# Kernel optimization log

Hardware: AMD Instinct MI355X
Metric: run time of the kernel (lower is better)

Reference implementation:

```python
import jax, jax.numpy as jnp
import numpy as np

B, T, C, H = 8, 2048, 1024, 128  # batch, seq (== block_size), n_embd, head_size


def setup_inputs() -> dict:
    key = jax.random.key(0)
    ks = jax.random.split(key, 4)
    s = 1.0 / np.sqrt(C)  # keep logits sane for softmax
    return {
        "embedded_data": jax.random.normal(ks[0], (B, T, C), dtype=jnp.float32),
        "Wq": jax.random.normal(ks[1], (C, H), dtype=jnp.float32) * s,
        "bq": jnp.zeros((H,), dtype=jnp.float32),
        "Wk": jax.random.normal(ks[2], (C, H), dtype=jnp.float32) * s,
        "bk": jnp.zeros((H,), dtype=jnp.float32),
        "Wv": jax.random.normal(ks[3], (C, H), dtype=jnp.float32) * s,
        "bv": jnp.zeros((H,), dtype=jnp.float32),
    }


def reference(embedded_data, Wq, bq, Wk, bk, Wv, bv):
    Bc, Tc, Cc = embedded_data.shape
    q = embedded_data @ Wq + bq                      # [B,T,H]
    k = embedded_data @ Wk + bk                      # [B,T,H]
    v = embedded_data @ Wv + bv                      # [B,T,H]
    # NOTE: source scales by C**-0.5 (input embed dim), not head_size**-0.5
    wei = jnp.einsum("bqh,bkh->bqk", q, k) * (Cc ** -0.5)  # [B,T,T]
    causal = jnp.tril(jnp.ones((Tc, Tc), dtype=bool))
    wei = jnp.where(causal, wei, -jnp.inf)
    wei = jax.nn.softmax(wei, axis=-1)
    # dropout(p=0.2) is identity in eval mode
    out = jnp.einsum("bqk,bkh->bqh", wei, v)         # [B,T,H]
    return out
```

## Files before the change

kernel.cpp:

```cpp
#include <hip/hip_runtime.h>
#include <cstdint>
#include <cstddef>

typedef __bf16 bf16x8 __attribute__((ext_vector_type(8)));
typedef float f32x4 __attribute__((ext_vector_type(4)));

#define B_ 8
#define T_ 2048
#define C_ 1024
#define H_ 128

#define QSC 0.045084220027780106f

__device__ __forceinline__ unsigned short f2bf(float f) {
    __bf16 h = (__bf16)f;
    return *(unsigned short*)&h;
}
__device__ __forceinline__ float bf2f(unsigned short u) {
    union { unsigned int i; float f; } x; x.i = ((unsigned int)u) << 16;
    return x.f;
}

__device__ __forceinline__ void gload16(void* lds, const void* g) {
    __builtin_amdgcn_global_load_lds(
        (const __attribute__((address_space(1))) unsigned int*)g,
        (__attribute__((address_space(3))) unsigned int*)lds, 16, 0, 0);
}

__global__ __launch_bounds__(256) void prep_w(
    const float* __restrict__ Wq, const float* __restrict__ Wk,
    const float* __restrict__ Wv, unsigned short* __restrict__ wt)
{
    int gid = blockIdx.x * 256 + threadIdx.x;
    int which = gid >> 14;
    int rem = gid & 16383;
    int n = rem >> 7;
    int kc = rem & 127;
    const float* W = which == 0 ? Wq : (which == 1 ? Wk : Wv);
    unsigned short tmp[8];
    #pragma unroll
    for (int i = 0; i < 8; ++i) tmp[i] = f2bf(W[(size_t)(kc * 8 + i) * H_ + n]);
    *(uint4*)&wt[((size_t)which * H_ + n) * C_ + kc * 8] = *(uint4*)tmp;
}

__global__ __launch_bounds__(256, 2) void proj_fused5(
    const float* __restrict__ x, const unsigned short* __restrict__ wt,
    const float* __restrict__ bq, const float* __restrict__ bk,
    const float* __restrict__ bv,
    unsigned short* __restrict__ qo, unsigned short* __restrict__ ko,
    unsigned short* __restrict__ vo)
{
    __shared__ unsigned short smem[32768];

    const int tid = threadIdx.x;
    const int w = tid >> 6, l = tid & 63, gl = l >> 4, lc = l & 15;
    const int cb = w * 48;
    const int fam = blockIdx.y;
    const int m0 = blockIdx.x * 64;
    const unsigned short* wbase = wt + (size_t)fam * 192 * C_;

    const int sr = tid >> 2, q4 = tid & 3;
    const float* xrow = &x[(size_t)(m0 + sr) * C_ + q4 * 16];
    unsigned short* xw0;
    unsigned short* xw1;
    {
        int c0 = q4 * 2;
        (void)c0;
    }

    f32x4 acc[4][3];
    #pragma unroll
    for (int im = 0; im < 4; ++im)
        #pragma unroll
        for (int jn = 0; jn < 3; ++jn) acc[im][jn] = f32x4{0.f, 0.f, 0.f, 0.f};

    float xr[16];
    auto load_x = [&](int kc2) {
        const float* p = xrow + kc2 * 64;
        #pragma unroll
        for (int i = 0; i < 4; ++i) {
            float4 v4 = *(const float4*)(p + 4 * i);
            xr[4 * i + 0] = v4.x; xr[4 * i + 1] = v4.y;
            xr[4 * i + 2] = v4.z; xr[4 * i + 3] = v4.w;
        }
    };
    auto write_x = [&](int buf) {
        unsigned short tb[16];
        #pragma unroll
        for (int i = 0; i < 16; ++i) tb[i] = f2bf(xr[i]);
        unsigned short* xb = smem + buf * 4096;
        const int c0 = q4 * 2;
        *(uint4*)&xb[(sr * 8 + ((c0 + 0) ^ (sr & 7))) * 8] = *(uint4*)&tb[0];
        *(uint4*)&xb[(sr * 8 + ((c0 + 1) ^ (sr & 7))) * 8] = *(uint4*)&tb[8];
    };
    auto stage_w = [&](int buf, int kc2) {
        const int kb = kc2 * 64;
        unsigned short* wb = smem + 8192 + buf * 12288;
        #pragma unroll
        for (int ji = 0; ji < 6; ++ji) {
            int slot = ji * 256 + tid;
            int R = slot >> 3, cs = slot & 7;
            gload16(&wb[(ji * 256 + w * 64) * 8],
                    &wbase[(size_t)R * C_ + kb + ((cs ^ (R & 7)) * 8)]);
        }
    };

    load_x(0);
    stage_w(0, 0);
    asm volatile("s_waitcnt vmcnt(6)" ::: "memory");
    __builtin_amdgcn_sched_barrier(0);
    write_x(0);
    load_x(1);
    stage_w(1, 1);
    asm volatile("s_waitcnt vmcnt(10)" ::: "memory");
    __builtin_amdgcn_sched_barrier(0);
    asm volatile("s_waitcnt lgkmcnt(0)" ::: "memory");
    __builtin_amdgcn_sched_barrier(0);
    __builtin_amdgcn_s_barrier();

    for (int kc = 0; kc < 16; ++kc) {
        const int cur = kc & 1, nxt = cur ^ 1;
        const unsigned short* xb = smem + cur * 4096;
        const unsigned short* wb = smem + 8192 + cur * 12288;
        #pragma unroll
        for (int ks = 0; ks < 2; ++ks) {
            bf16x8 a[4], b[3];
            const int u = ks * 4 + gl;
            #pragma unroll
            for (int im = 0; im < 4; ++im) {
                int row = im * 16 + lc;
                a[im] = *(const bf16x8*)&xb[(row * 8 + (u ^ (lc & 7))) * 8];
            }
            #pragma unroll
            for (int jn = 0; jn < 3; ++jn) {
                int R = cb + jn * 16 + lc;
                b[jn] = *(const bf16x8*)&wb[(R * 8 + (u ^ (lc & 7))) * 8];
            }
            #pragma unroll
            for (int im = 0; im < 4; ++im)
                #pragma unroll
                for (int jn = 0; jn < 3; ++jn)
                    acc[im][jn] = __builtin_amdgcn_mfma_f32_16x16x32_bf16(
                        a[im], b[jn], acc[im][jn], 0, 0, 0);
        }
        __builtin_amdgcn_s_barrier();
        if (kc < 14) {
            asm volatile("s_waitcnt vmcnt(6)" ::: "memory");
            __builtin_amdgcn_sched_barrier(0);
            write_x(nxt);
            load_x(kc + 2);
            stage_w(cur, kc + 2);
            asm volatile("s_waitcnt vmcnt(10)" ::: "memory");
            __builtin_amdgcn_sched_barrier(0);
            asm volatile("s_waitcnt lgkmcnt(0)" ::: "memory");
            __builtin_amdgcn_sched_barrier(0);
            __builtin_amdgcn_s_barrier();
        } else if (kc == 14) {
            asm volatile("s_waitcnt vmcnt(6)" ::: "memory");
            __builtin_amdgcn_sched_barrier(0);
            write_x(nxt);
            asm volatile("s_waitcnt vmcnt(0)" ::: "memory");
            __builtin_amdgcn_sched_barrier(0);
            asm volatile("s_waitcnt lgkmcnt(0)" ::: "memory");
            __builtin_amdgcn_sched_barrier(0);
            __builtin_amdgcn_s_barrier();
        }
    }

    unsigned short* eb = smem;
    #pragma unroll
    for (int jn = 0; jn < 3; ++jn) {
        int nl_ = cb + jn * 16 + lc;
        int ng = fam * 192 + nl_;
        int wh = ng >> 7, nn = ng & 127;
        float bb = (wh == 0) ? bq[nn] : (wh == 1 ? bk[nn] : bv[nn]);
        float sc = (wh == 0) ? QSC : 1.0f;
        #pragma unroll
        for (int im = 0; im < 4; ++im)
            #pragma unroll
            for (int r = 0; r < 4; ++r) {
                int row = im * 16 + gl * 4 + r;
                eb[row * 200 + nl_] = f2bf((acc[im][jn][r] + bb) * sc);
            }
    }
    __syncthreads();

    const int bi = m0 >> 11, t0 = m0 & (T_ - 1);
    if (fam == 0) {
        #pragma unroll
        for (int i = 0; i < 4; ++i) {
            int c = i * 256 + tid;
            int row = c >> 4, c16 = c & 15;
            *(uint4*)&qo[(size_t)(m0 + row) * H_ + c16 * 8] =
                *(const uint4*)&eb[row * 200 + c16 * 8];
        }
        #pragma unroll
        for (int i = 0; i < 2; ++i) {
            int c = i * 256 + tid;
            int row = c >> 3, c8 = c & 7;
            *(uint4*)&ko[(size_t)(m0 + row) * H_ + c8 * 8] =
                *(const uint4*)&eb[row * 200 + 128 + c8 * 8];
        }
    } else {
        #pragma unroll
        for (int i = 0; i < 2; ++i) {
            int c = i * 256 + tid;
            int row = c >> 3, c8 = c & 7;
            *(uint4*)&ko[(size_t)(m0 + row) * H_ + 64 + c8 * 8] =
                *(const uint4*)&eb[row * 200 + c8 * 8];
        }
        #pragma unroll
        for (int i = 0; i < 4; ++i) {
            int c = i * 256 + tid;
            int n = c >> 3, cc = c & 7;
            unsigned short tmp[8];
            #pragma unroll
            for (int ii = 0; ii < 8; ++ii)
                tmp[ii] = eb[(cc * 8 + ii) * 200 + 64 + n];
            *(uint4*)&vo[((size_t)(bi * H_ + n)) * T_ + t0 + cc * 8] = *(uint4*)tmp;
        }
    }
}

__device__ __forceinline__ int pasc(int qt) {
    int m = qt >> 2, j = qt & 3;
    return 2 * m * (m + 1) + j * (m + 1);
}

__global__ __launch_bounds__(256, 2) void attn_split7(
    const unsigned short* __restrict__ q,
    const unsigned short* __restrict__ k,
    const unsigned short* __restrict__ vT,
    float* __restrict__ out,
    unsigned short* __restrict__ Opart, float* __restrict__ lws)
{
    const int bb = blockIdx.x;
    const int jj = 143 - (int)blockIdx.y;
    int qt = 31;
    while (pasc(qt) > jj) --qt;
    const int c = jj - pasc(qt);
    const int nch = (qt >> 2) + 1;
    const int q0 = qt * 64;
    const int kstart = c * 256;
    const int kend = min(kstart + 256, q0 + 64);
    const int ntiles = (kend - kstart) >> 5;

    const unsigned short* qb = q  + (size_t)bb * T_ * H_;
    const unsigned short* kb = k  + (size_t)bb * T_ * H_;
    const unsigned short* vb = vT + (size_t)bb * H_ * T_;

    __shared__ unsigned short Ks[2][32 * 128];
    __shared__ unsigned short Vs[2][128 * 32];
    __shared__ unsigned short Ps[4][16 * 64];

    const int tid = threadIdx.x;
    const int w = tid >> 6, l = tid & 63, gl = l >> 4, lc = l & 15;
    const int rowbase = q0 + w * 16;

    bf16x8 aq[4];
    #pragma unroll
    for (int ds = 0; ds < 4; ++ds)
        aq[ds] = *(const bf16x8*)&qb[(size_t)(rowbase + lc) * H_ + ds * 32 + gl * 8];

    f32x4 o[8];
    #pragma unroll
    for (int jo = 0; jo < 8; ++jo) o[jo] = f32x4{0.f, 0.f, 0.f, 0.f};
    float l_acc[4];
    #pragma unroll
    for (int r = 0; r < 4; ++r) l_acc[r] = 0.f;

    auto stageK = [&](int buf, int t) {
        const int kv0 = kstart + t * 32;
        #pragma unroll
        for (int ji = 0; ji < 2; ++ji) {
            int slot = (w * 2 + ji) * 64 + l;
            int r = slot >> 4, cs = slot & 15;
            gload16(&Ks[buf][((w * 2 + ji) * 64) * 8],
                    &kb[(size_t)(kv0 + r) * H_ + ((cs ^ (r & 7)) * 8)]);
        }
    };
    auto stageV = [&](int buf, int t) {
        const int kv0 = kstart + t * 32;
        #pragma unroll
        for (int ji = 0; ji < 2; ++ji) {
            int slot = (w * 2 + ji) * 64 + l;
            int r = slot >> 2, cs = slot & 3;
            gload16(&Vs[buf][((w * 2 + ji) * 64) * 8],
                    &vb[(size_t)r * T_ + kv0 + ((cs ^ (r & 3)) * 8)]);
        }
    };

    stageK(0, 0);
    stageV(0, 0);
    __syncthreads();

    int cur = 0;
    for (int t = 0; t < ntiles; ++t) {
        if (t + 1 < ntiles) { stageK(cur ^ 1, t + 1); stageV(cur ^ 1, t + 1); }
        const int kv0 = kstart + t * 32;
        const bool active = kv0 < rowbase + 16;
        if (active) {
            f32x4 s[2];
            #pragma unroll
            for (int jk = 0; jk < 2; ++jk) s[jk] = f32x4{0.f, 0.f, 0.f, 0.f};
            #pragma unroll
            for (int ds = 0; ds < 4; ++ds) {
                #pragma unroll
                for (int jk = 0; jk < 2; ++jk) {
                    int row = jk * 16 + lc;
                    bf16x8 kf = *(const bf16x8*)&Ks[cur][(row * 16 + ((ds * 4 + gl) ^ (row & 7))) * 8];
                    s[jk] = __builtin_amdgcn_mfma_f32_16x16x32_bf16(aq[ds], kf, s[jk], 0, 0, 0);
                }
            }
            if (kv0 + 31 > rowbase) {
                #pragma unroll
                for (int jk = 0; jk < 2; ++jk)
                    #pragma unroll
                    for (int r = 0; r < 4; ++r)
                        if (kv0 + jk * 16 + lc > rowbase + gl * 4 + r) s[jk][r] = -1e30f;
            }
            #pragma unroll
            for (int jk = 0; jk < 2; ++jk)
                #pragma unroll
                for (int r = 0; r < 4; ++r) {
                    float p = exp2f(fminf(s[jk][r], 80.f));
                    s[jk][r] = p;
                    l_acc[r] += p;
                }
            #pragma unroll
            for (int jk = 0; jk < 2; ++jk)
                #pragma unroll
                for (int r = 0; r < 4; ++r) {
                    int row = gl * 4 + r;
                    Ps[w][(row * 64 + jk * 16 + lc) ^ ((row & 7) << 3)] = f2bf(s[jk][r]);
                }
            {
                bf16x8 pa = *(const bf16x8*)&Ps[w][(lc * 64 + gl * 8) ^ ((lc & 7) << 3)];
                #pragma unroll
                for (int jo = 0; jo < 8; ++jo) {
                    int d = jo * 16 + lc;
                    bf16x8 vf = *(const bf16x8*)&Vs[cur][(d * 4 + (gl ^ (d & 3))) * 8];
                    o[jo] = __builtin_amdgcn_mfma_f32_16x16x32_bf16(pa, vf, o[jo], 0, 0, 0);
                }
            }
        }
        __syncthreads();
        cur ^= 1;
    }

    #pragma unroll
    for (int off = 1; off < 16; off <<= 1)
        #pragma unroll
        for (int r = 0; r < 4; ++r)
            l_acc[r] += __shfl_xor(l_acc[r], off, 64);

    if (nch == 1) {
        float* ob = out + (size_t)bb * T_ * H_;
        float inv[4];
        #pragma unroll
        for (int r = 0; r < 4; ++r) inv[r] = 1.0f / l_acc[r];
        #pragma unroll
        for (int jo = 0; jo < 8; ++jo)
            #pragma unroll
            for (int r = 0; r < 4; ++r)
                ob[(size_t)(rowbase + gl * 4 + r) * H_ + jo * 16 + lc] = o[jo][r] * inv[r];
    } else {
        const int slot = bb * 140 + (pasc(qt) - 4 + c);
        unsigned short* op = Opart + (size_t)slot * 8192;
        #pragma unroll
        for (int jo = 0; jo < 8; ++jo)
            #pragma unroll
            for (int r = 0; r < 4; ++r)
                op[(w * 16 + gl * 4 + r) * 128 + jo * 16 + lc] = f2bf(o[jo][r]);
        if (lc == 0) {
            #pragma unroll
            for (int r = 0; r < 4; ++r)
                lws[slot * 64 + w * 16 + gl * 4 + r] = l_acc[r];
        }
    }
}

__global__ __launch_bounds__(256) void combine_kernel(
    const unsigned short* __restrict__ Opart, const float* __restrict__ lws,
    float* __restrict__ out)
{
    const int rowid = blockIdx.x * 4 + (threadIdx.x >> 6);
    const int lane = threadIdx.x & 63;
    const int bb = rowid / 1792;
    const int t = 256 + (rowid - bb * 1792);
    const int qt = t >> 6;
    const int m = qt >> 2;
    const int nch = m + 1;
    const int p0 = 2 * m * (m + 1) + (qt & 3) * (m + 1);
    const int base = bb * 140 + (p0 - 4);
    const int r64 = t & 63;

    float L = 0.f, a0 = 0.f, a1 = 0.f;
    #pragma unroll
    for (int c2 = 0; c2 < 8; ++c2)
        if (c2 < nch) {
            L += lws[(base + c2) * 64 + r64];
            ushort2 uv = *(const ushort2*)&Opart[(size_t)(base + c2) * 8192 + r64 * 128 + lane * 2];
            a0 += bf2f(uv.x); a1 += bf2f(uv.y);
        }
    const float invL = 1.0f / L;
    *(float2*)&out[((size_t)bb * T_ + t) * H_ + lane * 2] = make_float2(a0 * invL, a1 * invL);
}

__global__ __launch_bounds__(128) void attn_mono(
    const unsigned short* __restrict__ q,
    const unsigned short* __restrict__ k,
    const unsigned short* __restrict__ vT,
    float* __restrict__ out)
{
    const int qt = (gridDim.x - 1) - blockIdx.x;
    const int bb = blockIdx.y;
    const int q0 = qt * 32;
    const unsigned short* qb = q  + (size_t)bb * T_ * H_;
    const unsigned short* kb = k  + (size_t)bb * T_ * H_;
    const unsigned short* vb = vT + (size_t)bb * H_ * T_;

    __shared__ unsigned short Ps[2][16 * 64];

    const int tid = threadIdx.x;
    const int w = tid >> 6, l = tid & 63, gl = l >> 4, lc = l & 15;

    bf16x8 aq[4];
    #pragma unroll
    for (int ds = 0; ds < 4; ++ds)
        aq[ds] = *(const bf16x8*)&qb[(size_t)(q0 + w * 16 + lc) * H_ + ds * 32 + gl * 8];

    f32x4 o[8];
    #pragma unroll
    for (int jo = 0; jo < 8; ++jo) o[jo] = f32x4{0.f, 0.f, 0.f, 0.f};
    float m_run[4], l_run[4];
    #pragma unroll
    for (int r = 0; r < 4; ++r) { m_run[r] = -INFINITY; l_run[r] = 0.f; }

    const int nt = (q0 >> 6) + 1;
    for (int t = 0; t < nt; ++t) {
        const int kv0 = t * 64;
        f32x4 s[4];
        #pragma unroll
        for (int jk = 0; jk < 4; ++jk) s[jk] = f32x4{0.f, 0.f, 0.f, 0.f};
        #pragma unroll
        for (int ds = 0; ds < 4; ++ds)
            #pragma unroll
            for (int jk = 0; jk < 4; ++jk) {
                bf16x8 bf = *(const bf16x8*)&kb[(size_t)(kv0 + jk * 16 + lc) * H_ + ds * 32 + gl * 8];
                s[jk] = __builtin_amdgcn_mfma_f32_16x16x32_bf16(aq[ds], bf, s[jk], 0, 0, 0);
            }
        if (kv0 + 63 > q0) {
            const int rowg = q0 + w * 16 + gl * 4;
            #pragma unroll
            for (int jk = 0; jk < 4; ++jk)
                #pragma unroll
                for (int r = 0; r < 4; ++r)
                    if (kv0 + jk * 16 + lc > rowg + r) s[jk][r] = -1e30f;
        }
        float pm[4];
        #pragma unroll
        for (int r = 0; r < 4; ++r)
            pm[r] = fmaxf(fmaxf(s[0][r], s[1][r]), fmaxf(s[2][r], s[3][r]));
        #pragma unroll
        for (int off = 1; off < 16; off <<= 1)
            #pragma unroll
            for (int r = 0; r < 4; ++r)
                pm[r] = fmaxf(pm[r], __shfl_xor(pm[r], off, 64));
        float scl[4], rs[4];
        #pragma unroll
        for (int r = 0; r < 4; ++r) {
            float mn = fmaxf(m_run[r], pm[r]);
            scl[r] = exp2f(m_run[r] - mn);
            m_run[r] = mn;
            rs[r] = 0.f;
        }
        #pragma unroll
        for (int jk = 0; jk < 4; ++jk)
            #pragma unroll
            for (int r = 0; r < 4; ++r) {
                float p = exp2f(s[jk][r] - m_run[r]);
                s[jk][r] = p;
                rs[r] += p;
            }
        #pragma unroll
        for (int off = 1; off < 16; off <<= 1)
            #pragma unroll
            for (int r = 0; r < 4; ++r)
                rs[r] += __shfl_xor(rs[r], off, 64);
        #pragma unroll
        for (int r = 0; r < 4; ++r)
            l_run[r] = l_run[r] * scl[r] + rs[r];
        #pragma unroll
        for (int jo = 0; jo < 8; ++jo)
            #pragma unroll
            for (int r = 0; r < 4; ++r)
                o[jo][r] *= scl[r];
        #pragma unroll
        for (int jk = 0; jk < 4; ++jk)
            #pragma unroll
            for (int r = 0; r < 4; ++r) {
                int row = gl * 4 + r;
                Ps[w][(row * 64 + jk * 16 + lc) ^ ((row & 7) << 3)] = f2bf(s[jk][r]);
            }
        #pragma unroll
        for (int ks = 0; ks < 2; ++ks) {
            bf16x8 pa = *(const bf16x8*)&Ps[w][(lc * 64 + ks * 32 + gl * 8) ^ ((lc & 7) << 3)];
            #pragma unroll
            for (int jo = 0; jo < 8; ++jo) {
                bf16x8 bv_ = *(const bf16x8*)&vb[(size_t)(jo * 16 + lc) * T_ + kv0 + ks * 32 + gl * 8];
                o[jo] = __builtin_amdgcn_mfma_f32_16x16x32_bf16(pa, bv_, o[jo], 0, 0, 0);
            }
        }
    }
    float* ob = out + (size_t)bb * T_ * H_;
    #pragma unroll
    for (int jo = 0; jo < 8; ++jo)
        #pragma unroll
        for (int r = 0; r < 4; ++r)
            ob[(size_t)(q0 + w * 16 + gl * 4 + r) * H_ + jo * 16 + lc] = o[jo][r] / l_run[r];
}

extern "C" void kernel_launch(void* const* d_in, const int* in_sizes, int n_in,
                              void* d_out, int out_size, void* d_ws, size_t ws_size,
                              hipStream_t stream) {
    const float* x  = (const float*)d_in[0];
    const float* Wq = (const float*)d_in[1];
    const float* bq = (const float*)d_in[2];
    const float* Wk = (const float*)d_in[3];
    const float* bk = (const float*)d_in[4];
    const float* Wv = (const float*)d_in[5];
    const float* bv = (const float*)d_in[6];
    float* out = (float*)d_out;

    const size_t qkv = (size_t)B_ * T_ * H_;
    unsigned short* qws = (unsigned short*)d_ws;
    unsigned short* kws = qws + qkv;
    unsigned short* vws = kws + qkv;
    unsigned short* wtw = vws + qkv;
    const size_t base_bytes = (3 * qkv + (size_t)3 * H_ * C_) * 2;
    unsigned short* Opart = (unsigned short*)((char*)d_ws + base_bytes);
    float* lws = (float*)((char*)d_ws + base_bytes + (size_t)1120 * 8192 * 2);
    const size_t need = base_bytes + (size_t)1120 * 8192 * 2 + (size_t)1120 * 64 * 4;

    prep_w<<<dim3(192), 256, 0, stream>>>(Wq, Wk, Wv, wtw);
    proj_fused5<<<dim3(256, 2), 256, 0, stream>>>(x, wtw, bq, bk, bv, qws, kws, vws);
    if (ws_size >= need) {
        attn_split7<<<dim3(8, 144), 256, 0, stream>>>(qws, kws, vws, out, Opart, lws);
        combine_kernel<<<dim3(3584), 256, 0, stream>>>(Opart, lws, out);
    } else {
        attn_mono<<<dim3(64, 8), 128, 0, stream>>>(qws, kws, vws, out);
    }
}
```

Baseline: 69.31 us.

## Split QKV projection into one 128-column block per Q/K/V family

```diff
diff --git a/kernel.cpp b/kernel.cpp
--- a/kernel.cpp
+++ b/kernel.cpp
@@ -43,36 +43,30 @@
     *(uint4*)&wt[((size_t)which * H_ + n) * C_ + kc * 8] = *(uint4*)tmp;
 }
 
-__global__ __launch_bounds__(256, 2) void proj_fused5(
+__global__ __launch_bounds__(256, 3) void proj_fused6(
     const float* __restrict__ x, const unsigned short* __restrict__ wt,
     const float* __restrict__ bq, const float* __restrict__ bk,
     const float* __restrict__ bv,
     unsigned short* __restrict__ qo, unsigned short* __restrict__ ko,
     unsigned short* __restrict__ vo)
 {
-    __shared__ unsigned short smem[32768];
+    __shared__ unsigned short smem[24576];
 
     const int tid = threadIdx.x;
     const int w = tid >> 6, l = tid & 63, gl = l >> 4, lc = l & 15;
-    const int cb = w * 48;
-    const int fam = blockIdx.y;
-    const int m0 = blockIdx.x * 64;
-    const unsigned short* wbase = wt + (size_t)fam * 192 * C_;
+    const int cb = w * 32;
+    const int fam = blockIdx.x;
+    const int m0 = blockIdx.y * 64;
+    const unsigned short* wbase = wt + (size_t)fam * H_ * C_;
 
     const int sr = tid >> 2, q4 = tid & 3;
     const float* xrow = &x[(size_t)(m0 + sr) * C_ + q4 * 16];
-    unsigned short* xw0;
-    unsigned short* xw1;
-    {
-        int c0 = q4 * 2;
-        (void)c0;
-    }
-
-    f32x4 acc[4][3];
+
+    f32x4 acc[4][2];
     #pragma unroll
     for (int im = 0; im < 4; ++im)
         #pragma unroll
-        for (int jn = 0; jn < 3; ++jn) acc[im][jn] = f32x4{0.f, 0.f, 0.f, 0.f};
+        for (int jn = 0; jn < 2; ++jn) acc[im][jn] = f32x4{0.f, 0.f, 0.f, 0.f};
 
     float xr[16];
     auto load_x = [&](int kc2) {
@@ -95,9 +89,9 @@
     };
     auto stage_w = [&](int buf, int kc2) {
         const int kb = kc2 * 64;
-        unsigned short* wb = smem + 8192 + buf * 12288;
-        #pragma unroll
-        for (int ji = 0; ji < 6; ++ji) {
+        unsigned short* wb = smem + 8192 + buf * 8192;
+        #pragma unroll
+        for (int ji = 0; ji < 4; ++ji) {
             int slot = ji * 256 + tid;
             int R = slot >> 3, cs = slot & 7;
             gload16(&wb[(ji * 256 + w * 64) * 8],
@@ -107,12 +101,12 @@
 
     load_x(0);
     stage_w(0, 0);
-    asm volatile("s_waitcnt vmcnt(6)" ::: "memory");
+    asm volatile("s_waitcnt vmcnt(4)" ::: "memory");
     __builtin_amdgcn_sched_barrier(0);
     write_x(0);
     load_x(1);
     stage_w(1, 1);
-    asm volatile("s_waitcnt vmcnt(10)" ::: "memory");
+    asm volatile("s_waitcnt vmcnt(8)" ::: "memory");
     __builtin_amdgcn_sched_barrier(0);
     asm volatile("s_waitcnt lgkmcnt(0)" ::: "memory");
     __builtin_amdgcn_sched_barrier(0);
@@ -121,10 +115,10 @@
     for (int kc = 0; kc < 16; ++kc) {
         const int cur = kc & 1, nxt = cur ^ 1;
         const unsigned short* xb = smem + cur * 4096;
-        const unsigned short* wb = smem + 8192 + cur * 12288;
+        const unsigned short* wb = smem + 8192 + cur * 8192;
         #pragma unroll
         for (int ks = 0; ks < 2; ++ks) {
-            bf16x8 a[4], b[3];
+            bf16x8 a[4], b[2];
             const int u = ks * 4 + gl;
             #pragma unroll
             for (int im = 0; im < 4; ++im) {
@@ -132,31 +126,31 @@
                 a[im] = *(const bf16x8*)&xb[(row * 8 + (u ^ (lc & 7))) * 8];
             }
             #pragma unroll
-            for (int jn = 0; jn < 3; ++jn) {
+            for (int jn = 0; jn < 2; ++jn) {
                 int R = cb + jn * 16 + lc;
                 b[jn] = *(const bf16x8*)&wb[(R * 8 + (u ^ (lc & 7))) * 8];
             }
             #pragma unroll
             for (int im = 0; im < 4; ++im)
                 #pragma unroll
-                for (int jn = 0; jn < 3; ++jn)
+                for (int jn = 0; jn < 2; ++jn)
                     acc[im][jn] = __builtin_amdgcn_mfma_f32_16x16x32_bf16(
                         a[im], b[jn], acc[im][jn], 0, 0, 0);
         }
         __builtin_amdgcn_s_barrier();
         if (kc < 14) {
-            asm volatile("s_waitcnt vmcnt(6)" ::: "memory");
+            asm volatile("s_waitcnt vmcnt(4)" ::: "memory");
             __builtin_amdgcn_sched_barrier(0);
             write_x(nxt);
             load_x(kc + 2);
             stage_w(cur, kc + 2);
-            asm volatile("s_waitcnt vmcnt(10)" ::: "memory");
+            asm volatile("s_waitcnt vmcnt(8)" ::: "memory");
             __builtin_amdgcn_sched_barrier(0);
             asm volatile("s_waitcnt lgkmcnt(0)" ::: "memory");
             __builtin_amdgcn_sched_barrier(0);
             __builtin_amdgcn_s_barrier();
         } else if (kc == 14) {
-            asm volatile("s_waitcnt vmcnt(6)" ::: "memory");
+            asm volatile("s_waitcnt vmcnt(4)" ::: "memory");
             __builtin_amdgcn_sched_barrier(0);
             write_x(nxt);
             asm volatile("s_waitcnt vmcnt(0)" ::: "memory");
@@ -168,47 +162,33 @@
     }
 
     unsigned short* eb = smem;
-    #pragma unroll
-    for (int jn = 0; jn < 3; ++jn) {
-        int nl_ = cb + jn * 16 + lc;
-        int ng = fam * 192 + nl_;
-        int wh = ng >> 7, nn = ng & 127;
-        float bb = (wh == 0) ? bq[nn] : (wh == 1 ? bk[nn] : bv[nn]);
-        float sc = (wh == 0) ? QSC : 1.0f;
+    const float* bias = fam == 0 ? bq : (fam == 1 ? bk : bv);
+    const float sc = (fam == 0) ? QSC : 1.0f;
+    #pragma unroll
+    for (int jn = 0; jn < 2; ++jn) {
+        int n = cb + jn * 16 + lc;
+        float bb = bias[n];
         #pragma unroll
         for (int im = 0; im < 4; ++im)
             #pragma unroll
             for (int r = 0; r < 4; ++r) {
                 int row = im * 16 + gl * 4 + r;
-                eb[row * 200 + nl_] = f2bf((acc[im][jn][r] + bb) * sc);
+                eb[row * 136 + n] = f2bf((acc[im][jn][r] + bb) * sc);
             }
     }
     __syncthreads();
 
     const int bi = m0 >> 11, t0 = m0 & (T_ - 1);
-    if (fam == 0) {
+    if (fam != 2) {
+        unsigned short* o = fam == 0 ? qo : ko;
         #pragma unroll
         for (int i = 0; i < 4; ++i) {
             int c = i * 256 + tid;
             int row = c >> 4, c16 = c & 15;
-            *(uint4*)&qo[(size_t)(m0 + row) * H_ + c16 * 8] =
-                *(const uint4*)&eb[row * 200 + c16 * 8];
-        }
-        #pragma unroll
-        for (int i = 0; i < 2; ++i) {
-            int c = i * 256 + tid;
-            int row = c >> 3, c8 = c & 7;
-            *(uint4*)&ko[(size_t)(m0 + row) * H_ + c8 * 8] =
-                *(const uint4*)&eb[row * 200 + 128 + c8 * 8];
+            *(uint4*)&o[(size_t)(m0 + row) * H_ + c16 * 8] =
+                *(const uint4*)&eb[row * 136 + c16 * 8];
         }
     } else {
-        #pragma unroll
-        for (int i = 0; i < 2; ++i) {
-            int c = i * 256 + tid;
-            int row = c >> 3, c8 = c & 7;
-            *(uint4*)&ko[(size_t)(m0 + row) * H_ + 64 + c8 * 8] =
-                *(const uint4*)&eb[row * 200 + c8 * 8];
-        }
         #pragma unroll
         for (int i = 0; i < 4; ++i) {
             int c = i * 256 + tid;
@@ -216,7 +196,7 @@
             unsigned short tmp[8];
             #pragma unroll
             for (int ii = 0; ii < 8; ++ii)
-                tmp[ii] = eb[(cc * 8 + ii) * 200 + 64 + n];
+                tmp[ii] = eb[(cc * 8 + ii) * 136 + n];
             *(uint4*)&vo[((size_t)(bi * H_ + n)) * T_ + t0 + cc * 8] = *(uint4*)tmp;
         }
     }
@@ -544,7 +524,7 @@
     const size_t need = base_bytes + (size_t)1120 * 8192 * 2 + (size_t)1120 * 64 * 4;
 
     prep_w<<<dim3(192), 256, 0, stream>>>(Wq, Wk, Wv, wtw);
-    proj_fused5<<<dim3(256, 2), 256, 0, stream>>>(x, wtw, bq, bk, bv, qws, kws, vws);
+    proj_fused6<<<dim3(3, 256), 256, 0, stream>>>(x, wtw, bq, bk, bv, qws, kws, vws);
     if (ws_size >= need) {
         attn_split7<<<dim3(8, 144), 256, 0, stream>>>(qws, kws, vws, out, Opart, lws);
         combine_kernel<<<dim3(3584), 256, 0, stream>>>(Opart, lws, out);
```

Result: slower. 80.20 us (+15.7%).
